# Kernel tuning notes

Hardware: AMD Instinct MI355X
Metric: run time of the kernel (lower is better)

Reference implementation:

```python
import jax, jax.numpy as jnp
import numpy as np

N = 50000   # nodes
R = 4       # relation groups
E = 800000  # nnz per relation adjacency
ED = 200000 # decoded edges
H = 128     # hidden_dim
L = 64      # latent_dim
DH = 64     # decoder_hidden_dim


def setup_inputs() -> dict:
    key = jax.random.key(0)
    ks = iter(jax.random.split(key, 64))
    def nrm(shape, scale=1.0):
        return jax.random.normal(next(ks), shape, dtype=jnp.float32) * scale
    inp = {}
    inp["x_process"] = nrm((N, 62))
    inp["x_file"] = nrm((N, 37))
    inp["x_network"] = nrm((N, 37))
    def lin(prefix, din, dout):
        s = 1.0 / np.sqrt(din)
        inp[prefix + "_Ws"] = nrm((dout, din), s)
        inp[prefix + "_bs"] = nrm((dout,), s)
        inp[prefix + "_Wr"] = nrm((R, dout, din), s)
        inp[prefix + "_br"] = nrm((R, dout), s)
    lin("p1", 62, H); lin("p2", H, L)
    lin("f1", 37, H); lin("f2", H, L)
    lin("n1", 37, H); lin("n2", H, L)
    inp["gate_W"] = nrm((3, L), 1.0 / np.sqrt(L))
    inp["gate_b"] = nrm((3,), 0.1)
    inp["dec_W1"] = nrm((DH, 4 * L), 1.0 / np.sqrt(4 * L))
    inp["dec_b1"] = nrm((DH,), 0.1)
    inp["dec_W2"] = nrm((1, DH), 1.0 / np.sqrt(DH))
    inp["dec_b2"] = nrm((1,), 0.1)
    inp["adj_rows"] = jax.random.randint(next(ks), (R, E), 0, N, dtype=jnp.int32)
    inp["adj_cols"] = jax.random.randint(next(ks), (R, E), 0, N, dtype=jnp.int32)
    inp["adj_vals"] = jax.random.uniform(next(ks), (R, E), dtype=jnp.float32) * 0.1
    inp["edge_src"] = jax.random.randint(next(ks), (ED,), 0, N, dtype=jnp.int32)
    inp["edge_dst"] = jax.random.randint(next(ks), (ED,), 0, N, dtype=jnp.int32)
    return inp


def reference(x_process, x_file, x_network,
              p1_Ws, p1_bs, p1_Wr, p1_br, p2_Ws, p2_bs, p2_Wr, p2_br,
              f1_Ws, f1_bs, f1_Wr, f1_br, f2_Ws, f2_bs, f2_Wr, f2_br,
              n1_Ws, n1_bs, n1_Wr, n1_br, n2_Ws, n2_bs, n2_Wr, n2_br,
              gate_W, gate_b, dec_W1, dec_b1, dec_W2, dec_b2,
              adj_rows, adj_cols, adj_vals, edge_src, edge_dst):
    def spmm(rows, cols, vals, x):  # A @ x, A in COO: out[row] += val * x[col]
        return jax.ops.segment_sum(vals[:, None] * x[cols], rows, num_segments=N)

    def rgcn_layer(x, Ws, bs, Wr, br):
        out = x @ Ws.T + bs  # self_linear
        for r in range(R):
            out = out + spmm(adj_rows[r], adj_cols[r], adj_vals[r], x) @ Wr[r].T + br[r]
        return out / float(R + 1)

    def encoder(x, W1s, b1s, W1r, b1r, W2s, b2s, W2r, b2r):
        h = jax.nn.relu(rgcn_layer(x, W1s, b1s, W1r, b1r))
        # dropout p=0.0 / eval mode -> identity
        return rgcn_layer(h, W2s, b2s, W2r, b2r)

    z_p = encoder(x_process, p1_Ws, p1_bs, p1_Wr, p1_br, p2_Ws, p2_bs, p2_Wr, p2_br)
    z_f = encoder(x_file, f1_Ws, f1_bs, f1_Wr, f1_br, f2_Ws, f2_bs, f2_Wr, f2_br)
    z_n = encoder(x_network, n1_Ws, n1_bs, n1_Wr, n1_br, n2_Ws, n2_bs, n2_Wr, n2_br)

    # gated multi-view fusion: three Linear(latent,1) gates -> softmax over views
    scores = jnp.stack([z_p @ gate_W[0] + gate_b[0],
                        z_f @ gate_W[1] + gate_b[1],
                        z_n @ gate_W[2] + gate_b[2]], axis=1)  # [N, 3]
    alpha = jax.nn.softmax(scores, axis=1)
    z = alpha[:, 0:1] * z_p + alpha[:, 1:2] * z_f + alpha[:, 2:3] * z_n  # [N, L]

    # mlp edge decoder
    zs = z[edge_src]
    zd = z[edge_dst]
    feats = jnp.concatenate([zs, zd, zs * zd, jnp.abs(zs - zd)], axis=1)  # [ED, 4L]
    hid = jax.nn.relu(feats @ dec_W1.T + dec_b1)
    logits = (hid @ dec_W2.T + dec_b2)[:, 0]  # [ED]
    return logits
```

## Files before the change

### kernel.cpp

```cpp
#include <hip/hip_runtime.h>

#define N_NODES 50000
#define R_REL   4
#define E_NNZ   800000
#define ED_EDGES 200000
#define H_DIM   128
#define L_DIM   64

#define RN_TOTAL (R_REL * N_NODES)
#define ETOT     (R_REL * E_NNZ)

#define EPB   8192
#define NB    391
#define RBK   196
#define KBK   (R_REL * RBK)
#define HTOT  (KBK * NB)
#define SCB   300
#define MAXB  6144

#define WS_RP    0u
#define WS_HIST  800256u
#define WS_BSUM  2026496u
#define WS_BIAS3 2028544u
#define WS_CV    2030592u
#define WS_YALL  27630720u
#define WS_TMP   27630720u
#define WS_PART  27630720u
#define WS_SF    53230720u
#define WS_SN    82830720u
#define WS_XALL  112430720u
#define WS_YSP   112430720u
#define WS_SP    131630720u
#define WS_HF    131630720u
#define WS_YSN   131630720u
#define WS_HN    157230720u
#define WS_HPR   188001536u
#define WS_YSF   188001536u
#define WS_Z     200801536u

__device__ __forceinline__ ushort f2bf(float f) {
    unsigned u = __float_as_uint(f);
    unsigned r = (u + 0x7fffu + ((u >> 16) & 1u)) >> 16;
    return (ushort)r;
}
__device__ __forceinline__ float bf2f(ushort u) {
    return __uint_as_float(((unsigned)u) << 16);
}

__global__ void cast_xall_kernel(const float* __restrict__ xp, const float* __restrict__ xf,
                                 const float* __restrict__ xn, ushort* __restrict__ xall) {
    int i = blockIdx.x * 256 + threadIdx.x;
    if (i >= N_NODES * 192) return;
    int node = i / 192, k = i - node * 192;
    float v = 0.f;
    if (k < 62) v = xp[node * 62 + k];
    else if (k >= 64 && k < 138) {
        int j = k - 64, d = j >> 1;
        v = (j & 1) ? xn[node * 37 + d] : xf[node * 37 + d];
    }
    xall[i] = f2bf(v);
}

__global__ void radix_hist_kernel(const int* __restrict__ rows, int* __restrict__ H) {
    __shared__ int hist[KBK];
    int blk = blockIdx.x, t = threadIdx.x;
    for (int i = t; i < KBK; i += 256) hist[i] = 0;
    __syncthreads();
    int base = blk * EPB;
    #pragma unroll 1
    for (int i = 0; i < EPB / 256; i++) {
        int g = base + i * 256 + t;
        if (g < ETOT) {
            int r = g / E_NNZ;
            atomicAdd(&hist[r * RBK + (rows[g] >> 8)], 1);
        }
    }
    __syncthreads();
    for (int i = t; i < KBK; i += 256) H[i * NB + blk] = hist[i];
}

__global__ void scan_part_kernel(const int* __restrict__ H, int* __restrict__ bsum) {
    __shared__ int red[256];
    int base = blockIdx.x * 1024, t = threadIdx.x;
    int s = 0;
    #pragma unroll
    for (int i = 0; i < 4; i++) {
        int idx = base + i * 256 + t;
        if (idx < HTOT) s += H[idx];
    }
    red[t] = s; __syncthreads();
    for (int d = 128; d > 0; d >>= 1) {
        if (t < d) red[t] += red[t + d];
        __syncthreads();
    }
    if (t == 0) bsum[blockIdx.x] = red[0];
}

__global__ void scan_bsum_kernel(int* __restrict__ bsum, int* __restrict__ rp) {
    __shared__ int sh[512];
    int t = threadIdx.x;
    int v = (t < SCB) ? bsum[t] : 0;
    sh[t] = v; __syncthreads();
    for (int d = 1; d < 512; d <<= 1) {
        int u = (t >= d) ? sh[t - d] : 0;
        __syncthreads();
        sh[t] += u;
        __syncthreads();
    }
    if (t < SCB) bsum[t] = sh[t] - v;
    if (t == 0) rp[RN_TOTAL] = ETOT;
}

__global__ void scan_final_kernel(int* __restrict__ H, const int* __restrict__ bsum) {
    __shared__ int sh[256];
    int base = blockIdx.x * 1024, t = threadIdx.x;
    int c[4]; int s = 0;
    #pragma unroll
    for (int i = 0; i < 4; i++) {
        int idx = base + t * 4 + i;
        c[i] = (idx < HTOT) ? H[idx] : 0;
        s += c[i];
    }
    sh[t] = s; __syncthreads();
    for (int d = 1; d < 256; d <<= 1) {
        int u = (t >= d) ? sh[t - d] : 0;
        __syncthreads();
        sh[t] += u;
        __syncthreads();
    }
    int off = bsum[blockIdx.x] + sh[t] - s;
    #pragma unroll
    for (int i = 0; i < 4; i++) {
        int idx = base + t * 4 + i;
        if (idx < HTOT) H[idx] = off;
        off += c[i];
    }
}

__global__ void radix_scatter_kernel(const int* __restrict__ rows, const int* __restrict__ cols,
                                     const float* __restrict__ vals, const int* __restrict__ H,
                                     int2* __restrict__ tmp) {
    __shared__ int cur[KBK];
    int blk = blockIdx.x, t = threadIdx.x;
    for (int i = t; i < KBK; i += 256) cur[i] = H[i * NB + blk];
    __syncthreads();
    int base = blk * EPB;
    #pragma unroll 1
    for (int i = 0; i < EPB / 256; i++) {
        int g = base + i * 256 + t;
        if (g < ETOT) {
            int r = g / E_NNZ;
            int row = rows[g];
            int b = r * RBK + (row >> 8);
            int p = atomicAdd(&cur[b], 1);
            tmp[p] = make_int2(cols[g] | ((row & 255) << 16), __float_as_int(vals[g]));
        }
    }
}

__launch_bounds__(256)
__global__ void bucket_sort_kernel(const int2* __restrict__ tmp, const int* __restrict__ H,
                                   int* __restrict__ rp, int2* __restrict__ cse) {
    __shared__ int hist[256];
    __shared__ int sc[256];
    __shared__ int cur[256];
    __shared__ int2 eb[MAXB];
    int b = blockIdx.x, t = threadIdx.x;
    int start = H[b * NB];
    int end = (b == KBK - 1) ? ETOT : H[(b + 1) * NB];
    int cnt = end - start;
    bool useLds = (cnt <= MAXB);
    hist[t] = 0;
    __syncthreads();
    for (int i = t; i < cnt; i += 256) {
        int2 e = tmp[start + i];
        if (useLds) eb[i] = e;
        atomicAdd(&hist[(e.x >> 16) & 255], 1);
    }
    __syncthreads();
    sc[t] = hist[t]; __syncthreads();
    for (int d = 1; d < 256; d <<= 1) {
        int v = (t >= d) ? sc[t - d] : 0;
        __syncthreads();
        sc[t] += v;
        __syncthreads();
    }
    int pref = sc[t] - hist[t];
    int r = b / RBK, rh = b - r * RBK;
    int grow = rh * 256 + t;
    if (grow < N_NODES) rp[r * N_NODES + grow] = start + pref;
    cur[t] = start + pref;
    __syncthreads();
    for (int i = t; i < cnt; i += 256) {
        int2 e = useLds ? eb[i] : tmp[start + i];
        int rl = (e.x >> 16) & 255;
        int p = atomicAdd(&cur[rl], 1);
        cse[p] = make_int2(e.x & 0xFFFF, e.y);
    }
}

__global__ void spmm1_all_kernel(const ushort* __restrict__ xall,
                                 const int* __restrict__ rp, const int2* __restrict__ cse,
                                 float* __restrict__ Sp, float* __restrict__ Sf,
                                 float* __restrict__ Sn) {
    int wave = threadIdx.x >> 6, lane = threadIdx.x & 63;
    int row = blockIdx.x * 4 + wave;
    if (row >= N_NODES) return;
    int h = lane >> 5, j = lane & 31;
    unsigned d0 = 2u * (unsigned)j;
    unsigned po = d0;
    unsigned fo = 64u + 2u * d0;
    for (int r = 0; r < R_REL; r++) {
        int e0 = rp[r * N_NODES + row], e1 = rp[r * N_NODES + row + 1];
        float ap0 = 0.f, ap1 = 0.f, af0 = 0.f, af1 = 0.f, an0 = 0.f, an1 = 0.f;
        int e = e0;
        for (; e + 8 <= e1; e += 8) {
            int2 qA = cse[e + h],     qB = cse[e + 2 + h];
            int2 qC = cse[e + 4 + h], qD = cse[e + 6 + h];
            unsigned bA = (unsigned)qA.x * 192u, bB = (unsigned)qB.x * 192u;
            unsigned bC = (unsigned)qC.x * 192u, bD = (unsigned)qD.x * 192u;
            ushort2 pA = *(const ushort2*)(xall + bA + po);
            ushort2 pB = *(const ushort2*)(xall + bB + po);
            ushort2 pC = *(const ushort2*)(xall + bC + po);
            ushort2 pD = *(const ushort2*)(xall + bD + po);
            ushort4 uA = *(const ushort4*)(xall + bA + fo);
            ushort4 uB = *(const ushort4*)(xall + bB + fo);
            ushort4 uC = *(const ushort4*)(xall + bC + fo);
            ushort4 uD = *(const ushort4*)(xall + bD + fo);
            float vA = __int_as_float(qA.y), vB = __int_as_float(qB.y);
            float vC = __int_as_float(qC.y), vD = __int_as_float(qD.y);
            ap0 += vA * bf2f(pA.x) + vB * bf2f(pB.x) + vC * bf2f(pC.x) + vD * bf2f(pD.x);
            ap1 += vA * bf2f(pA.y) + vB * bf2f(pB.y) + vC * bf2f(pC.y) + vD * bf2f(pD.y);
            af0 += vA * bf2f(uA.x) + vB * bf2f(uB.x) + vC * bf2f(uC.x) + vD * bf2f(uD.x);
            an0 += vA * bf2f(uA.y) + vB * bf2f(uB.y) + vC * bf2f(uC.y) + vD * bf2f(uD.y);
            af1 += vA * bf2f(uA.z) + vB * bf2f(uB.z) + vC * bf2f(uC.z) + vD * bf2f(uD.z);
            an1 += vA * bf2f(uA.w) + vB * bf2f(uB.w) + vC * bf2f(uC.w) + vD * bf2f(uD.w);
        }
        for (; e < e1; e += 2) {
            int idx = e + h;
            int2 q = cse[idx < e1 ? idx : e1 - 1];
            float v = (idx < e1) ? __int_as_float(q.y) : 0.f;
            unsigned b = (unsigned)q.x * 192u;
            ushort2 p = *(const ushort2*)(xall + b + po);
            ushort4 u = *(const ushort4*)(xall + b + fo);
            ap0 += v * bf2f(p.x); ap1 += v * bf2f(p.y);
            af0 += v * bf2f(u.x); an0 += v * bf2f(u.y);
            af1 += v * bf2f(u.z); an1 += v * bf2f(u.w);
        }
        ap0 += __shfl_xor(ap0, 32); ap1 += __shfl_xor(ap1, 32);
        af0 += __shfl_xor(af0, 32); af1 += __shfl_xor(af1, 32);
        an0 += __shfl_xor(an0, 32); an1 += __shfl_xor(an1, 32);
        if (h == 0) {
            int d = (int)d0;
            if (d < 62) *(float2*)(Sp + row * 248 + r * 62 + d) = make_float2(ap0, ap1);
            float* sfp = Sf + row * 148 + r * 37;
            float* snp = Sn + row * 148 + r * 37;
            if (d < 37) { sfp[d] = af0; snp[d] = an0; }
            if (d < 36) { sfp[d + 1] = af1; snp[d + 1] = an1; }
        }
    }
}

__launch_bounds__(256)
__global__ void gemm1_kernel(const float* __restrict__ x, const float* __restrict__ S,
                             const float* __restrict__ Ws, const float* __restrict__ bs,
                             const float* __restrict__ Wr, const float* __restrict__ br,
                             float* __restrict__ h, int din) {
    __shared__ float sA[64 * 63];
    __shared__ float sW[62 * 132];
    int t = threadIdx.x;
    int i0 = blockIdx.x * 64;
    int rg = t >> 5, cg = t & 31;
    float acc[8][4] = {};
    for (int s = 0; s < 5; s++) {
        const float* Aptr; int astride;
        if (s == 0) { Aptr = x; astride = din; }
        else        { Aptr = S + (s - 1) * din; astride = 4 * din; }
        const float* Wp = (s == 0) ? Ws : (Wr + (s - 1) * H_DIM * din);
        __syncthreads();
        for (int idx = t; idx < 64 * din; idx += 256) {
            int rr = idx / din, k = idx - rr * din;
            int grow = i0 + rr;
            sA[rr * 63 + k] = (grow < N_NODES) ? Aptr[grow * astride + k] : 0.f;
        }
        for (int idx = t; idx < H_DIM * din; idx += 256) {
            int j = idx / din, k = idx - j * din;
            sW[k * 132 + j] = Wp[j * din + k];
        }
        __syncthreads();
        for (int k = 0; k < din; k++) {
            float a[8];
            #pragma unroll
            for (int rr = 0; rr < 8; rr++) a[rr] = sA[(rg * 8 + rr) * 63 + k];
            float4 w = *(const float4*)&sW[k * 132 + cg * 4];
            #pragma unroll
            for (int rr = 0; rr < 8; rr++) {
                acc[rr][0] += a[rr] * w.x; acc[rr][1] += a[rr] * w.y;
                acc[rr][2] += a[rr] * w.z; acc[rr][3] += a[rr] * w.w;
            }
        }
    }
    int j0 = cg * 4;
    float btot[4];
    #pragma unroll
    for (int cc = 0; cc < 4; cc++) {
        float b = bs[j0 + cc];
        #pragma unroll
        for (int r = 0; r < R_REL; r++) b += br[r * H_DIM + j0 + cc];
        btot[cc] = b;
    }
    #pragma unroll
    for (int rr = 0; rr < 8; rr++) {
        int grow = i0 + rg * 8 + rr;
        if (grow < N_NODES) {
            float4 o;
            o.x = fmaxf((acc[rr][0] + btot[0]) * 0.2f, 0.f);
            o.y = fmaxf((acc[rr][1] + btot[1]) * 0.2f, 0.f);
            o.z = fmaxf((acc[rr][2] + btot[2]) * 0.2f, 0.f);
            o.w = fmaxf((acc[rr][3] + btot[3]) * 0.2f, 0.f);
            *(float4*)&h[grow * H_DIM + j0] = o;
        }
    }
}

__launch_bounds__(256)
__global__ void gemm2_kernel(const float* __restrict__ h, const float* __restrict__ Ws2,
                             const float* __restrict__ Wr2, float* __restrict__ Yself,
                             ushort* __restrict__ Yall, int view) {
    __shared__ float sA[128 * 65];
    __shared__ float sW[64 * 68];
    int t = threadIdx.x;
    int i0 = blockIdx.x * 128;
    int ct = blockIdx.y;
    int rg = t >> 4, cg = t & 15;
    const float* Wp = (ct == 0) ? Ws2 : (Wr2 + (ct - 1) * 64 * H_DIM);
    float acc[8][4] = {};
    for (int kc = 0; kc < 2; kc++) {
        __syncthreads();
        for (int idx = t; idx < 128 * 64; idx += 256) {
            int rr = idx >> 6, k = idx & 63;
            int grow = i0 + rr;
            sA[rr * 65 + k] = (grow < N_NODES) ? h[grow * H_DIM + kc * 64 + k] : 0.f;
        }
        for (int idx = t; idx < 64 * 64; idx += 256) {
            int j = idx >> 6, k = idx & 63;
            sW[k * 68 + j] = Wp[j * H_DIM + kc * 64 + k];
        }
        __syncthreads();
        for (int k = 0; k < 64; k++) {
            float a[8];
            #pragma unroll
            for (int rr = 0; rr < 8; rr++) a[rr] = sA[(rg * 8 + rr) * 65 + k];
            float4 w = *(const float4*)&sW[k * 68 + cg * 4];
            #pragma unroll
            for (int rr = 0; rr < 8; rr++) {
                acc[rr][0] += a[rr] * w.x; acc[rr][1] += a[rr] * w.y;
                acc[rr][2] += a[rr] * w.z; acc[rr][3] += a[rr] * w.w;
            }
        }
    }
    #pragma unroll
    for (int rr = 0; rr < 8; rr++) {
        int grow = i0 + rg * 8 + rr;
        if (grow < N_NODES) {
            if (ct == 0) {
                float4 o = make_float4(acc[rr][0], acc[rr][1], acc[rr][2], acc[rr][3]);
                *(float4*)&Yself[(size_t)grow * 64 + cg * 4] = o;
            } else {
                ushort4 o;
                o.x = f2bf(acc[rr][0]); o.y = f2bf(acc[rr][1]);
                o.z = f2bf(acc[rr][2]); o.w = f2bf(acc[rr][3]);
                *(ushort4*)&Yall[(size_t)grow * 768 + (ct - 1) * 192 + view * 64 + cg * 4] = o;
            }
        }
    }
}

__global__ void bias_prep_kernel(const float* __restrict__ pbs, const float* __restrict__ pbr,
                                 const float* __restrict__ fbs, const float* __restrict__ fbr,
                                 const float* __restrict__ nbs, const float* __restrict__ nbr,
                                 float* __restrict__ bias3) {
    int t = threadIdx.x;
    if (t >= 192) return;
    int view = t >> 6, d = t & 63;
    const float* bs = (view == 0) ? pbs : (view == 1) ? fbs : nbs;
    const float* br = (view == 0) ? pbr : (view == 1) ? fbr : nbr;
    float b = bs[d];
    #pragma unroll
    for (int r = 0; r < R_REL; r++) b += br[r * 64 + d];
    bias3[t] = b;
}

__launch_bounds__(256)
__global__ void spmm2z_all_kernel(const float* __restrict__ Ysp,
                                  const float* __restrict__ Ysf,
                                  const float* __restrict__ Ysn,
                                  const ushort* __restrict__ Yall,
                                  const int* __restrict__ rp, const int2* __restrict__ cse,
                                  const float* __restrict__ bias3,
                                  const float* __restrict__ gW, const float* __restrict__ gb,
                                  float* __restrict__ z) {
    int wave = threadIdx.x >> 6, lane = threadIdx.x & 63;
    int row = blockIdx.x * 4 + wave;
    if (row >= N_NODES) return;
    int h = lane >> 5, j = lane & 31;
    unsigned d0 = 2u * (unsigned)j;
    float aP0 = 0.f, aP1 = 0.f, aF0 = 0.f, aF1 = 0.f, aN0 = 0.f, aN1 = 0.f;
    for (int r = 0; r < R_REL; r++) {
        int e0 = rp[r * N_NODES + row], e1 = rp[r * N_NODES + row + 1];
        unsigned ofs = (unsigned)(r * 192) + d0;
        int e = e0;
        for (; e + 8 <= e1; e += 8) {
            int2 qA = cse[e + h],     qB = cse[e + 2 + h];
            int2 qC = cse[e + 4 + h], qD = cse[e + 6 + h];
            unsigned oA = (unsigned)qA.x * 768u + ofs;
            unsigned oB = (unsigned)qB.x * 768u + ofs;
            unsigned oC = (unsigned)qC.x * 768u + ofs;
            unsigned oD = (unsigned)qD.x * 768u + ofs;
            ushort2 pA = *(const ushort2*)(Yall + oA);
            ushort2 fA = *(const ushort2*)(Yall + oA + 64);
            ushort2 nA = *(const ushort2*)(Yall + oA + 128);
            ushort2 pB = *(const ushort2*)(Yall + oB);
            ushort2 fB = *(const ushort2*)(Yall + oB + 64);
            ushort2 nB = *(const ushort2*)(Yall + oB + 128);
            ushort2 pC = *(const ushort2*)(Yall + oC);
            ushort2 fC = *(const ushort2*)(Yall + oC + 64);
            ushort2 nC = *(const ushort2*)(Yall + oC + 128);
            ushort2 pD = *(const ushort2*)(Yall + oD);
            ushort2 fD = *(const ushort2*)(Yall + oD + 64);
            ushort2 nD = *(const ushort2*)(Yall + oD + 128);
            float vA = __int_as_float(qA.y), vB = __int_as_float(qB.y);
            float vC = __int_as_float(qC.y), vD = __int_as_float(qD.y);
            aP0 += vA * bf2f(pA.x) + vB * bf2f(pB.x) + vC * bf2f(pC.x) + vD * bf2f(pD.x);
            aP1 += vA * bf2f(pA.y) + vB * bf2f(pB.y) + vC * bf2f(pC.y) + vD * bf2f(pD.y);
            aF0 += vA * bf2f(fA.x) + vB * bf2f(fB.x) + vC * bf2f(fC.x) + vD * bf2f(fD.x);
            aF1 += vA * bf2f(fA.y) + vB * bf2f(fB.y) + vC * bf2f(fC.y) + vD * bf2f(fD.y);
            aN0 += vA * bf2f(nA.x) + vB * bf2f(nB.x) + vC * bf2f(nC.x) + vD * bf2f(nD.x);
            aN1 += vA * bf2f(nA.y) + vB * bf2f(nB.y) + vC * bf2f(nC.y) + vD * bf2f(nD.y);
        }
        for (; e < e1; e += 2) {
            int idx = e + h;
            int2 q = cse[idx < e1 ? idx : e1 - 1];
            float v = (idx < e1) ? __int_as_float(q.y) : 0.f;
            unsigned o = (unsigned)q.x * 768u + ofs;
            ushort2 p = *(const ushort2*)(Yall + o);
            ushort2 f = *(const ushort2*)(Yall + o + 64);
            ushort2 n = *(const ushort2*)(Yall + o + 128);
            aP0 += v * bf2f(p.x); aP1 += v * bf2f(p.y);
            aF0 += v * bf2f(f.x); aF1 += v * bf2f(f.y);
            aN0 += v * bf2f(n.x); aN1 += v * bf2f(n.y);
        }
    }
    aP0 += __shfl_xor(aP0, 32); aP1 += __shfl_xor(aP1, 32);
    aF0 += __shfl_xor(aF0, 32); aF1 += __shfl_xor(aF1, 32);
    aN0 += __shfl_xor(aN0, 32); aN1 += __shfl_xor(aN1, 32);
    size_t rb = (size_t)row * 64 + d0;
    float2 ysp = *(const float2*)(Ysp + rb);
    float2 ysf = *(const float2*)(Ysf + rb);
    float2 ysn = *(const float2*)(Ysn + rb);
    aP0 = (aP0 + ysp.x + bias3[d0]) * 0.2f;
    aP1 = (aP1 + ysp.y + bias3[d0 + 1]) * 0.2f;
    aF0 = (aF0 + ysf.x + bias3[64 + d0]) * 0.2f;
    aF1 = (aF1 + ysf.y + bias3[64 + d0 + 1]) * 0.2f;
    aN0 = (aN0 + ysn.x + bias3[128 + d0]) * 0.2f;
    aN1 = (aN1 + ysn.y + bias3[128 + d0 + 1]) * 0.2f;
    float sp = aP0 * gW[d0] + aP1 * gW[d0 + 1];
    float sf = aF0 * gW[64 + d0] + aF1 * gW[64 + d0 + 1];
    float sn = aN0 * gW[128 + d0] + aN1 * gW[128 + d0 + 1];
    #pragma unroll
    for (int d = 16; d >= 1; d >>= 1) {
        sp += __shfl_xor(sp, d);
        sf += __shfl_xor(sf, d);
        sn += __shfl_xor(sn, d);
    }
    sp += gb[0]; sf += gb[1]; sn += gb[2];
    float m = fmaxf(sp, fmaxf(sf, sn));
    float ep = __expf(sp - m), ef = __expf(sf - m), en = __expf(sn - m);
    float inv = 1.f / (ep + ef + en);
    if (h == 0) {
        float2 zo;
        zo.x = (ep * aP0 + ef * aF0 + en * aN0) * inv;
        zo.y = (ep * aP1 + ef * aF1 + en * aN1) * inv;
        *(float2*)(z + rb) = zo;
    }
}

__launch_bounds__(256)
__global__ void decoder7_kernel(const float* __restrict__ z, const int* __restrict__ esrc,
                                const int* __restrict__ edst, const float* __restrict__ w1,
                                const float* __restrict__ b1, const float* __restrict__ w2,
                                float* __restrict__ part) {
    __shared__ float sW1[8192];
    int t = threadIdx.x;
    int jh = blockIdx.y;
    const float* w1h = w1 + jh * 32 * 256;
    for (int i = t; i < 2048; i += 256)
        ((float4*)sW1)[i] = ((const float4*)w1h)[i];
    __syncthreads();
    int e1 = blockIdx.x * 512 + t;
    int e2 = e1 + 256;
    bool v2 = e2 < ED_EDGES;
    if (e1 >= ED_EDGES) return;
    int s1 = esrc[e1], d1 = edst[e1];
    int s2 = v2 ? esrc[e2] : s1;
    int d2 = v2 ? edst[e2] : d1;
    const float4* zs1 = (const float4*)(z + (size_t)s1 * 64);
    const float4* zd1 = (const float4*)(z + (size_t)d1 * 64);
    const float4* zs2 = (const float4*)(z + (size_t)s2 * 64);
    const float4* zd2 = (const float4*)(z + (size_t)d2 * 64);
    float hid1[32], hid2[32];
    #pragma unroll
    for (int j = 0; j < 32; j++) { hid1[j] = 0.f; hid2[j] = 0.f; }
    #pragma unroll 1
    for (int kc = 0; kc < 16; kc++) {
        float4 a1 = zs1[kc], b1v4 = zd1[kc];
        float4 a2 = zs2[kc], b2v4 = zd2[kc];
        float4 p1, q1, p2, q2;
        p1.x = a1.x * b1v4.x; q1.x = fabsf(a1.x - b1v4.x);
        p1.y = a1.y * b1v4.y; q1.y = fabsf(a1.y - b1v4.y);
        p1.z = a1.z * b1v4.z; q1.z = fabsf(a1.z - b1v4.z);
        p1.w = a1.w * b1v4.w; q1.w = fabsf(a1.w - b1v4.w);
        p2.x = a2.x * b2v4.x; q2.x = fabsf(a2.x - b2v4.x);
        p2.y = a2.y * b2v4.y; q2.y = fabsf(a2.y - b2v4.y);
        p2.z = a2.z * b2v4.z; q2.z = fabsf(a2.z - b2v4.z);
        p2.w = a2.w * b2v4.w; q2.w = fabsf(a2.w - b2v4.w);
        const float* wb0 = sW1 + kc * 4;
        #pragma unroll
        for (int j = 0; j < 32; j++) {
            const float* wr = wb0 + j * 256;
            float4 wa = *(const float4*)(wr);
            float4 wbv = *(const float4*)(wr + 64);
            float4 wc = *(const float4*)(wr + 128);
            float4 wd = *(const float4*)(wr + 192);
            float s1ab = a1.x * wa.x + a1.y * wa.y + a1.z * wa.z + a1.w * wa.w
                       + b1v4.x * wbv.x + b1v4.y * wbv.y + b1v4.z * wbv.z + b1v4.w * wbv.w;
            float s1pq = p1.x * wc.x + p1.y * wc.y + p1.z * wc.z + p1.w * wc.w
                       + q1.x * wd.x + q1.y * wd.y + q1.z * wd.z + q1.w * wd.w;
            hid1[j] += s1ab + s1pq;
            float s2ab = a2.x * wa.x + a2.y * wa.y + a2.z * wa.z + a2.w * wa.w
                       + b2v4.x * wbv.x + b2v4.y * wbv.y + b2v4.z * wbv.z + b2v4.w * wbv.w;
            float s2pq = p2.x * wc.x + p2.y * wc.y + p2.z * wc.z + p2.w * wc.w
                       + q2.x * wd.x + q2.y * wd.y + q2.z * wd.z + q2.w * wd.w;
            hid2[j] += s2ab + s2pq;
        }
    }
    float lg1a = 0.f, lg1b = 0.f, lg2a = 0.f, lg2b = 0.f;
    #pragma unroll
    for (int j = 0; j < 32; j += 2) {
        int gj = jh * 32 + j;
        float bj0 = b1[gj], wj0 = w2[gj];
        float bj1 = b1[gj + 1], wj1 = w2[gj + 1];
        lg1a += fmaxf(hid1[j] + bj0, 0.f) * wj0;
        lg1b += fmaxf(hid1[j + 1] + bj1, 0.f) * wj1;
        lg2a += fmaxf(hid2[j] + bj0, 0.f) * wj0;
        lg2b += fmaxf(hid2[j + 1] + bj1, 0.f) * wj1;
    }
    part[(size_t)jh * ED_EDGES + e1] = lg1a + lg1b;
    if (v2) part[(size_t)jh * ED_EDGES + e2] = lg2a + lg2b;
}

__global__ void dec_combine_kernel(const float* __restrict__ part, const float* __restrict__ b2,
                                   float* __restrict__ out) {
    int e = blockIdx.x * 256 + threadIdx.x;
    if (e < ED_EDGES) out[e] = part[e] + part[ED_EDGES + e] + b2[0];
}

extern "C" void kernel_launch(void* const* d_in, const int* in_sizes, int n_in,
                              void* d_out, int out_size, void* d_ws, size_t ws_size,
                              hipStream_t stream) {
    const float* x_p = (const float*)d_in[0];
    const float* x_f = (const float*)d_in[1];
    const float* x_n = (const float*)d_in[2];
    const float* p1_Ws = (const float*)d_in[3];  const float* p1_bs = (const float*)d_in[4];
    const float* p1_Wr = (const float*)d_in[5];  const float* p1_br = (const float*)d_in[6];
    const float* p2_Ws = (const float*)d_in[7];  const float* p2_bs = (const float*)d_in[8];
    const float* p2_Wr = (const float*)d_in[9];  const float* p2_br = (const float*)d_in[10];
    const float* f1_Ws = (const float*)d_in[11]; const float* f1_bs = (const float*)d_in[12];
    const float* f1_Wr = (const float*)d_in[13]; const float* f1_br = (const float*)d_in[14];
    const float* f2_Ws = (const float*)d_in[15]; const float* f2_bs = (const float*)d_in[16];
    const float* f2_Wr = (const float*)d_in[17]; const float* f2_br = (const float*)d_in[18];
    const float* n1_Ws = (const float*)d_in[19]; const float* n1_bs = (const float*)d_in[20];
    const float* n1_Wr = (const float*)d_in[21]; const float* n1_br = (const float*)d_in[22];
    const float* n2_Ws = (const float*)d_in[23]; const float* n2_bs = (const float*)d_in[24];
    const float* n2_Wr = (const float*)d_in[25]; const float* n2_br = (const float*)d_in[26];
    const float* gate_W = (const float*)d_in[27]; const float* gate_b = (const float*)d_in[28];
    const float* dec_W1 = (const float*)d_in[29]; const float* dec_b1 = (const float*)d_in[30];
    const float* dec_W2 = (const float*)d_in[31]; const float* dec_b2 = (const float*)d_in[32];
    const int*   adj_rows = (const int*)d_in[33];
    const int*   adj_cols = (const int*)d_in[34];
    const float* adj_vals = (const float*)d_in[35];
    const int*   edge_src = (const int*)d_in[36];
    const int*   edge_dst = (const int*)d_in[37];

    char* ws = (char*)d_ws;
    int*    rp   = (int*)(ws + WS_RP);
    int*    H    = (int*)(ws + WS_HIST);
    int*    bsum = (int*)(ws + WS_BSUM);
    float*  bias3 = (float*)(ws + WS_BIAS3);
    int2*   cse  = (int2*)(ws + WS_CV);
    int2*   tmp  = (int2*)(ws + WS_TMP);
    ushort* xall = (ushort*)(ws + WS_XALL);
    ushort* Yall = (ushort*)(ws + WS_YALL);
    float*  S_p = (float*)(ws + WS_SP);
    float*  S_f = (float*)(ws + WS_SF);
    float*  S_n = (float*)(ws + WS_SN);
    float*  h_p = (float*)(ws + WS_HPR);
    float*  h_f = (float*)(ws + WS_HF);
    float*  h_n = (float*)(ws + WS_HN);
    float*  Ys_p = (float*)(ws + WS_YSP);
    float*  Ys_f = (float*)(ws + WS_YSF);
    float*  Ys_n = (float*)(ws + WS_YSN);
    float*  z    = (float*)(ws + WS_Z);
    float*  part = (float*)(ws + WS_PART);
    float*  out  = (float*)d_out;

    cast_xall_kernel<<<(N_NODES * 192 + 255) / 256, 256, 0, stream>>>(x_p, x_f, x_n, xall);

    radix_hist_kernel<<<NB, 256, 0, stream>>>(adj_rows, H);
    scan_part_kernel<<<SCB, 256, 0, stream>>>(H, bsum);
    scan_bsum_kernel<<<1, 512, 0, stream>>>(bsum, rp);
    scan_final_kernel<<<SCB, 256, 0, stream>>>(H, bsum);
    radix_scatter_kernel<<<NB, 256, 0, stream>>>(adj_rows, adj_cols, adj_vals, H, tmp);
    bucket_sort_kernel<<<KBK, 256, 0, stream>>>(tmp, H, rp, cse);

    spmm1_all_kernel<<<N_NODES / 4, 256, 0, stream>>>(xall, rp, cse, S_p, S_f, S_n);

    int g1 = (N_NODES + 63) / 64;
    gemm1_kernel<<<g1, 256, 0, stream>>>(x_p, S_p, p1_Ws, p1_bs, p1_Wr, p1_br, h_p, 62);
    gemm1_kernel<<<g1, 256, 0, stream>>>(x_f, S_f, f1_Ws, f1_bs, f1_Wr, f1_br, h_f, 37);
    gemm1_kernel<<<g1, 256, 0, stream>>>(x_n, S_n, n1_Ws, n1_bs, n1_Wr, n1_br, h_n, 37);

    dim3 g2((N_NODES + 127) / 128, 5);
    gemm2_kernel<<<g2, 256, 0, stream>>>(h_p, p2_Ws, p2_Wr, Ys_p, Yall, 0);
    gemm2_kernel<<<g2, 256, 0, stream>>>(h_f, f2_Ws, f2_Wr, Ys_f, Yall, 1);
    gemm2_kernel<<<g2, 256, 0, stream>>>(h_n, n2_Ws, n2_Wr, Ys_n, Yall, 2);

    bias_prep_kernel<<<1, 192, 0, stream>>>(p2_bs, p2_br, f2_bs, f2_br, n2_bs, n2_br, bias3);
    spmm2z_all_kernel<<<N_NODES / 4, 256, 0, stream>>>(
        Ys_p, Ys_f, Ys_n, Yall, rp, cse, bias3, gate_W, gate_b, z);

    dim3 gd((ED_EDGES + 511) / 512, 2);
    decoder7_kernel<<<gd, 256, 0, stream>>>(
        z, edge_src, edge_dst, dec_W1, dec_b1, dec_W2, part);
    dec_combine_kernel<<<(ED_EDGES + 255) / 256, 256, 0, stream>>>(part, dec_b2, out);
}
```

Baseline: 1.431 ms.

## Precompute per-node decoder projections for src/dst halves of first layer

Splits the decoder's first linear layer so the terms depending only on z[src] and z[dst] are computed once per node by a new small GEMM kernel, with the bias folded in. The per-edge kernel then only evaluates the product and absolute-difference terms and adds gathered per-node projections. This roughly halves per-edge FMAs and shared-weight traffic, at the cost of an extra kernel and extra random gathers of 128-float rows per endpoint.

Measured after the change: 1.406 ms. About the same (-1.7%).

```diff
diff --git a/kernel.cpp b/kernel.cpp
--- a/kernel.cpp
+++ b/kernel.cpp
@@ -26,6 +26,7 @@
 #define WS_YALL  27630720u
 #define WS_TMP   27630720u
 #define WS_PART  27630720u
+#define WS_UV    53230720u
 #define WS_SF    53230720u
 #define WS_SN    82830720u
 #define WS_XALL  112430720u
@@ -486,16 +487,64 @@
 }
 
 __launch_bounds__(256)
-__global__ void decoder7_kernel(const float* __restrict__ z, const int* __restrict__ esrc,
+__global__ void uvgemm_kernel(const float* __restrict__ z, const float* __restrict__ w1,
+                              const float* __restrict__ b1, float* __restrict__ uv) {
+    __shared__ float sA[128 * 65];
+    __shared__ float sW[64 * 68];
+    int t = threadIdx.x;
+    int i0 = blockIdx.x * 128;
+    int ct = blockIdx.y;
+    int rg = t >> 4, cg = t & 15;
+    for (int idx = t; idx < 128 * 64; idx += 256) {
+        int rr = idx >> 6, k = idx & 63;
+        int grow = i0 + rr;
+        sA[rr * 65 + k] = (grow < N_NODES) ? z[(size_t)grow * 64 + k] : 0.f;
+    }
+    for (int idx = t; idx < 64 * 64; idx += 256) {
+        int j = idx >> 6, k = idx & 63;
+        sW[k * 68 + j] = w1[j * 256 + ct * 64 + k];
+    }
+    __syncthreads();
+    float acc[8][4] = {};
+    for (int k = 0; k < 64; k++) {
+        float a[8];
+        #pragma unroll
+        for (int rr = 0; rr < 8; rr++) a[rr] = sA[(rg * 8 + rr) * 65 + k];
+        float4 w = *(const float4*)&sW[k * 68 + cg * 4];
+        #pragma unroll
+        for (int rr = 0; rr < 8; rr++) {
+            acc[rr][0] += a[rr] * w.x; acc[rr][1] += a[rr] * w.y;
+            acc[rr][2] += a[rr] * w.z; acc[rr][3] += a[rr] * w.w;
+        }
+    }
+    int j0 = cg * 4;
+    float4 bv = make_float4(0.f, 0.f, 0.f, 0.f);
+    if (ct == 0) {
+        bv.x = b1[j0]; bv.y = b1[j0 + 1]; bv.z = b1[j0 + 2]; bv.w = b1[j0 + 3];
+    }
+    #pragma unroll
+    for (int rr = 0; rr < 8; rr++) {
+        int grow = i0 + rg * 8 + rr;
+        if (grow < N_NODES) {
+            float4 o = make_float4(acc[rr][0] + bv.x, acc[rr][1] + bv.y,
+                                   acc[rr][2] + bv.z, acc[rr][3] + bv.w);
+            *(float4*)&uv[(size_t)grow * 128 + ct * 64 + j0] = o;
+        }
+    }
+}
+
+__launch_bounds__(256)
+__global__ void decoder8_kernel(const float* __restrict__ z, const int* __restrict__ esrc,
                                 const int* __restrict__ edst, const float* __restrict__ w1,
-                                const float* __restrict__ b1, const float* __restrict__ w2,
+                                const float* __restrict__ uv, const float* __restrict__ w2,
                                 float* __restrict__ part) {
-    __shared__ float sW1[8192];
+    __shared__ float sW1[4096];
     int t = threadIdx.x;
     int jh = blockIdx.y;
-    const float* w1h = w1 + jh * 32 * 256;
-    for (int i = t; i < 2048; i += 256)
-        ((float4*)sW1)[i] = ((const float4*)w1h)[i];
+    for (int i = t; i < 1024; i += 256) {
+        int j = i >> 5, c = i & 31;
+        ((float4*)sW1)[i] = *(const float4*)(w1 + (jh * 32 + j) * 256 + 128 + c * 4);
+    }
     __syncthreads();
     int e1 = blockIdx.x * 512 + t;
     int e2 = e1 + 256;
@@ -527,36 +576,37 @@
         const float* wb0 = sW1 + kc * 4;
         #pragma unroll
         for (int j = 0; j < 32; j++) {
-            const float* wr = wb0 + j * 256;
-            float4 wa = *(const float4*)(wr);
-            float4 wbv = *(const float4*)(wr + 64);
-            float4 wc = *(const float4*)(wr + 128);
-            float4 wd = *(const float4*)(wr + 192);
-            float s1ab = a1.x * wa.x + a1.y * wa.y + a1.z * wa.z + a1.w * wa.w
-                       + b1v4.x * wbv.x + b1v4.y * wbv.y + b1v4.z * wbv.z + b1v4.w * wbv.w;
-            float s1pq = p1.x * wc.x + p1.y * wc.y + p1.z * wc.z + p1.w * wc.w
-                       + q1.x * wd.x + q1.y * wd.y + q1.z * wd.z + q1.w * wd.w;
-            hid1[j] += s1ab + s1pq;
-            float s2ab = a2.x * wa.x + a2.y * wa.y + a2.z * wa.z + a2.w * wa.w
-                       + b2v4.x * wbv.x + b2v4.y * wbv.y + b2v4.z * wbv.z + b2v4.w * wbv.w;
-            float s2pq = p2.x * wc.x + p2.y * wc.y + p2.z * wc.z + p2.w * wc.w
-                       + q2.x * wd.x + q2.y * wd.y + q2.z * wd.z + q2.w * wd.w;
-            hid2[j] += s2ab + s2pq;
-        }
-    }
-    float lg1a = 0.f, lg1b = 0.f, lg2a = 0.f, lg2b = 0.f;
-    #pragma unroll
-    for (int j = 0; j < 32; j += 2) {
-        int gj = jh * 32 + j;
-        float bj0 = b1[gj], wj0 = w2[gj];
-        float bj1 = b1[gj + 1], wj1 = w2[gj + 1];
-        lg1a += fmaxf(hid1[j] + bj0, 0.f) * wj0;
-        lg1b += fmaxf(hid1[j + 1] + bj1, 0.f) * wj1;
-        lg2a += fmaxf(hid2[j] + bj0, 0.f) * wj0;
-        lg2b += fmaxf(hid2[j + 1] + bj1, 0.f) * wj1;
-    }
-    part[(size_t)jh * ED_EDGES + e1] = lg1a + lg1b;
-    if (v2) part[(size_t)jh * ED_EDGES + e2] = lg2a + lg2b;
+            const float* wr = wb0 + j * 128;
+            float4 wc = *(const float4*)(wr);
+            float4 wd = *(const float4*)(wr + 64);
+            hid1[j] += p1.x * wc.x + p1.y * wc.y + p1.z * wc.z + p1.w * wc.w
+                     + q1.x * wd.x + q1.y * wd.y + q1.z * wd.z + q1.w * wd.w;
+            hid2[j] += p2.x * wc.x + p2.y * wc.y + p2.z * wc.z + p2.w * wc.w
+                     + q2.x * wd.x + q2.y * wd.y + q2.z * wd.z + q2.w * wd.w;
+        }
+    }
+    const float4* U1 = (const float4*)(uv + (size_t)s1 * 128 + jh * 32);
+    const float4* V1 = (const float4*)(uv + (size_t)d1 * 128 + 64 + jh * 32);
+    const float4* U2 = (const float4*)(uv + (size_t)s2 * 128 + jh * 32);
+    const float4* V2 = (const float4*)(uv + (size_t)d2 * 128 + 64 + jh * 32);
+    float lg1 = 0.f, lg2 = 0.f;
+    #pragma unroll
+    for (int jj = 0; jj < 8; jj++) {
+        float4 u1 = U1[jj], vv1 = V1[jj];
+        float4 u2 = U2[jj], vv2 = V2[jj];
+        int gj = jh * 32 + jj * 4;
+        float w0 = w2[gj], w1v = w2[gj + 1], w2v = w2[gj + 2], w3v = w2[gj + 3];
+        lg1 += fmaxf(hid1[jj * 4]     + u1.x + vv1.x, 0.f) * w0
+             + fmaxf(hid1[jj * 4 + 1] + u1.y + vv1.y, 0.f) * w1v
+             + fmaxf(hid1[jj * 4 + 2] + u1.z + vv1.z, 0.f) * w2v
+             + fmaxf(hid1[jj * 4 + 3] + u1.w + vv1.w, 0.f) * w3v;
+        lg2 += fmaxf(hid2[jj * 4]     + u2.x + vv2.x, 0.f) * w0
+             + fmaxf(hid2[jj * 4 + 1] + u2.y + vv2.y, 0.f) * w1v
+             + fmaxf(hid2[jj * 4 + 2] + u2.z + vv2.z, 0.f) * w2v
+             + fmaxf(hid2[jj * 4 + 3] + u2.w + vv2.w, 0.f) * w3v;
+    }
+    part[(size_t)jh * ED_EDGES + e1] = lg1;
+    if (v2) part[(size_t)jh * ED_EDGES + e2] = lg2;
 }
 
 __global__ void dec_combine_kernel(const float* __restrict__ part, const float* __restrict__ b2,
@@ -611,6 +661,7 @@
     float*  Ys_f = (float*)(ws + WS_YSF);
     float*  Ys_n = (float*)(ws + WS_YSN);
     float*  z    = (float*)(ws + WS_Z);
+    float*  uv   = (float*)(ws + WS_UV);
     float*  part = (float*)(ws + WS_PART);
     float*  out  = (float*)d_out;
 
@@ -639,8 +690,11 @@
     spmm2z_all_kernel<<<N_NODES / 4, 256, 0, stream>>>(
         Ys_p, Ys_f, Ys_n, Yall, rp, cse, bias3, gate_W, gate_b, z);
 
+    dim3 guv((N_NODES + 127) / 128, 2);
+    uvgemm_kernel<<<guv, 256, 0, stream>>>(z, dec_W1, dec_b1, uv);
+
     dim3 gd((ED_EDGES + 511) / 512, 2);
-    decoder7_kernel<<<gd, 256, 0, stream>>>(
-        z, edge_src, edge_dst, dec_W1, dec_b1, dec_W2, part);
+    decoder8_kernel<<<gd, 256, 0, stream>>>(
+        z, edge_src, edge_dst, dec_W1, uv, dec_W2, part);
     dec_combine_kernel<<<(ED_EDGES + 255) / 256, 256, 0, stream>>>(part, dec_b2, out);
 }
```
